# Kernel optimization log

Measured on AMD Instinct MI355X. Metric: run time of the kernel, lower is better.

## Reference

```python
import jax, jax.numpy as jnp
import numpy as np

HEADS = 8
DIM_HEAD = 128
ATTN_MATRIX_SCALE = 1.5  # tau applied to mean-centered logits
SCALE = DIM_HEAD ** -0.5


def setup_inputs() -> dict:
    key = jax.random.key(0)
    ks = jax.random.split(key, 7)
    b, n, m = 2, 2048, 2048
    qd, cd, inner = 1024, 768, HEADS * DIM_HEAD
    x = jax.random.normal(ks[0], (b, n, qd), dtype=jnp.float32)
    context = jax.random.normal(ks[1], (b, m, cd), dtype=jnp.float32)
    Wq = jax.random.normal(ks[2], (qd, inner), dtype=jnp.float32) * (qd ** -0.5)
    Wk = jax.random.normal(ks[3], (cd, inner), dtype=jnp.float32) * (cd ** -0.5)
    Wv = jax.random.normal(ks[4], (cd, inner), dtype=jnp.float32) * (cd ** -0.5)
    Wout = jax.random.normal(ks[5], (inner, qd), dtype=jnp.float32) * (inner ** -0.5)
    bout = jnp.zeros((qd,), dtype=jnp.float32)
    return {"x": x, "context": context, "Wq": Wq, "Wk": Wk, "Wv": Wv,
            "Wout": Wout, "bout": bout}


def _split_heads(t):
    # (b, n, h*d) -> (h, b*n, d); matches rearrange '(b h) n d -> h (b n) d'
    b, n, _ = t.shape
    t = t.reshape(b, n, HEADS, DIM_HEAD)
    return t.transpose(2, 0, 1, 3).reshape(HEADS, b * n, DIM_HEAD)


def reference(x, context, Wq, Wk, Wv, Wout, bout):
    b, n, _ = x.shape
    qh = _split_heads(jnp.einsum('bnq,qi->bni', x, Wq))        # (h, b*n, d)
    kh = _split_heads(jnp.einsum('bmc,ci->bmi', context, Wk))  # (h, b*m, d)
    vh = _split_heads(jnp.einsum('bmc,ci->bmi', context, Wv))  # (h, b*m, d)

    # custom mean-centered / tau-scaled similarity (_compute_sim_with_tau)
    sim = jnp.einsum('hid,hjd->hij', qh, kh) * SCALE
    mean = jnp.mean(sim, axis=-1, keepdims=True)
    sim = (sim - mean) * ATTN_MATRIX_SCALE + mean

    attn = jax.nn.softmax(sim, axis=-1)
    out = jnp.einsum('hij,hjd->hid', attn, vh)                 # (h, b*n, d)

    # (h, b*n, d) -> (b, n, h*d)
    out = out.reshape(HEADS, b, n, DIM_HEAD).transpose(1, 2, 0, 3)
    out = out.reshape(b, n, HEADS * DIM_HEAD)
    return jnp.einsum('bni,iq->bnq', out, Wout) + bout
```

## Files before the change

kernel.cpp:

```cpp
#include <hip/hip_runtime.h>
#include <cstdint>
#include <cstddef>

typedef unsigned short u16t;
typedef __bf16 bf16x8_t __attribute__((ext_vector_type(8)));
typedef float f32x4_t __attribute__((ext_vector_type(4)));
typedef float f32x16_t __attribute__((ext_vector_type(16)));

#define MFMA_BF16 __builtin_amdgcn_mfma_f32_16x16x32_bf16
#define MFMA32    __builtin_amdgcn_mfma_f32_32x32x16_bf16

__device__ __forceinline__ u16t f2bf(float f) {
    uint32_t u = __builtin_bit_cast(uint32_t, f);
    u += 0x7fffu + ((u >> 16) & 1u);
    return (u16t)(u >> 16);
}

__device__ __forceinline__ uint32_t pk2bf(float a, float b) {
    return (uint32_t)f2bf(a) | ((uint32_t)f2bf(b) << 16);
}

__device__ __forceinline__ float bflo(uint32_t u) {
    return __builtin_bit_cast(float, u << 16);
}
__device__ __forceinline__ float bfhi(uint32_t u) {
    return __builtin_bit_cast(float, u & 0xffff0000u);
}

__device__ __forceinline__ bf16x8_t ld_frag(const u16t* p) {
    return __builtin_bit_cast(bf16x8_t, *(const uint4*)p);
}

__device__ __forceinline__ uint32_t cvtpk(float lo, float hi) {
    uint32_t r;
    asm("v_cvt_pk_bf16_f32 %0, %1, %2" : "=v"(r) : "v"(lo), "v"(hi));
    return r;
}
__device__ __forceinline__ void swap32(uint32_t& a, uint32_t& b) {
    asm("v_permlane32_swap_b32 %0, %1" : "+v"(a), "+v"(b));
}

__device__ __forceinline__ void gl_lds16(const u16t* g, u16t* l) {
    __builtin_amdgcn_global_load_lds(
        (const __attribute__((address_space(1))) void*)g,
        (__attribute__((address_space(3))) void*)l, 16, 0, 0);
}

__global__ void cast2_bf16_kernel(const float* __restrict__ s0, u16t* __restrict__ d0, int n0,
                                  const float* __restrict__ s1, u16t* __restrict__ d1, int n1) {
    int i = blockIdx.x * blockDim.x + threadIdx.x;
    const float* s; u16t* d;
    if (i < n0) { s = s0; d = d0; }
    else { i -= n0; if (i >= n1) return; s = s1; d = d1; }
    float4 v = ((const float4*)s)[i];
    uint2 o;
    o.x = pk2bf(v.x, v.y);
    o.y = pk2bf(v.z, v.w);
    ((uint2*)d)[i] = o;
}

__global__ void transpose4_kernel(const float* __restrict__ Wq, const float* __restrict__ Wk,
                                  const float* __restrict__ Wv, const float* __restrict__ Wo,
                                  u16t* __restrict__ Wqt, u16t* __restrict__ Wkt,
                                  u16t* __restrict__ Wvt, u16t* __restrict__ Wot) {
    const int z = blockIdx.z;
    const float* W = z == 0 ? Wq : (z == 1 ? Wk : (z == 2 ? Wv : Wo));
    u16t* Wt      = z == 0 ? Wqt : (z == 1 ? Wkt : (z == 2 ? Wvt : Wot));
    const int K   = (z == 1 || z == 2) ? 768 : 1024;
    const int N = 1024;
    int n0 = blockIdx.x * 32, k0 = blockIdx.y * 32;
    if (k0 >= K) return;
    __shared__ float tile[32][33];
    int tx = threadIdx.x, ty = threadIdx.y;
    for (int i = ty; i < 32; i += 8)
        tile[i][tx] = W[(size_t)(k0 + i) * N + n0 + tx];
    __syncthreads();
    for (int i = ty; i < 32; i += 8)
        Wt[(size_t)(n0 + i) * K + k0 + tx] = f2bf(tile[tx][i]);
}

__device__ __forceinline__ void gemm_core(
    const u16t* __restrict__ A, const u16t* __restrict__ Bt,
    int K, void* __restrict__ outp, const float* __restrict__ bias,
    int mode, float oscale, int bm, int bn)
{
    __shared__ __align__(16) u16t As[2][128 * 64];
    __shared__ __align__(16) u16t Bs[2][64 * 64];
    const int tid = threadIdx.x;
    const int wave = tid >> 6, lane = tid & 63;
    const int wm = wave & 1, wn = wave >> 1;
    const int quad = lane >> 4, l16 = lane & 15;

    const int l8r = lane >> 3, l8c = lane & 7;
    const int cgx = (l8c ^ l8r) * 8;

    f32x4_t acc[4][2];
#pragma unroll
    for (int i = 0; i < 4; ++i)
#pragma unroll
        for (int j = 0; j < 2; ++j) acc[i][j] = (f32x4_t){0.f, 0.f, 0.f, 0.f};

    const int nk = K >> 6;

#pragma unroll
    for (int it = 0; it < 4; ++it) {
        int rb = wave * 32 + it * 8;
        gl_lds16(&A[(size_t)(bm + rb + l8r) * K + cgx], &As[0][rb * 64]);
    }
#pragma unroll
    for (int it = 0; it < 2; ++it) {
        int rb = wave * 16 + it * 8;
        gl_lds16(&Bt[(size_t)(bn + rb + l8r) * K + cgx], &Bs[0][rb * 64]);
    }

    for (int ki = 0; ki < nk; ++ki) {
        const int buf = ki & 1;
        __syncthreads();

        if (ki + 1 < nk) {
            const int kc = (ki + 1) << 6;
#pragma unroll
            for (int it = 0; it < 4; ++it) {
                int rb = wave * 32 + it * 8;
                gl_lds16(&A[(size_t)(bm + rb + l8r) * K + kc + cgx], &As[buf ^ 1][rb * 64]);
            }
#pragma unroll
            for (int it = 0; it < 2; ++it) {
                int rb = wave * 16 + it * 8;
                gl_lds16(&Bt[(size_t)(bn + rb + l8r) * K + kc + cgx], &Bs[buf ^ 1][rb * 64]);
            }
        }

#pragma unroll
        for (int ks = 0; ks < 2; ++ks) {
            bf16x8_t af[4], bfv[2];
#pragma unroll
            for (int i = 0; i < 4; ++i) {
                int r = wm * 64 + i * 16 + l16;
                af[i] = ld_frag(&As[buf][r * 64 + (((ks * 4 + quad) ^ (r & 7)) * 8)]);
            }
#pragma unroll
            for (int j = 0; j < 2; ++j) {
                int r = wn * 32 + j * 16 + l16;
                bfv[j] = ld_frag(&Bs[buf][r * 64 + (((ks * 4 + quad) ^ (r & 7)) * 8)]);
            }
#pragma unroll
            for (int i = 0; i < 4; ++i)
#pragma unroll
                for (int j = 0; j < 2; ++j)
                    acc[i][j] = MFMA_BF16(af[i], bfv[j], acc[i][j], 0, 0, 0);
        }
    }

    if (mode == 3) {
        float* out = (float*)outp;
#pragma unroll
        for (int j = 0; j < 2; ++j) {
            int c = bn + wn * 32 + j * 16 + l16;
            float b = bias[c];
#pragma unroll
            for (int i = 0; i < 4; ++i) {
                int rb = bm + wm * 64 + i * 16 + quad * 4;
#pragma unroll
                for (int r = 0; r < 4; ++r)
                    out[(size_t)(rb + r) * 1024 + c] = acc[i][j][r] + b;
            }
        }
    }
}

__global__ __launch_bounds__(256) void gemm_bf16_kernel(
    const u16t* __restrict__ A, const u16t* __restrict__ Bt,
    int K, void* __restrict__ outp, const float* __restrict__ bias,
    int mode, float oscale)
{
    gemm_core(A, Bt, K, outp, bias, mode, oscale, blockIdx.y * 128, blockIdx.x * 64);
}

__global__ __launch_bounds__(256, 2) void qkv128_kernel(
    const u16t* __restrict__ x_bf, const u16t* __restrict__ ctx_bf,
    const u16t* __restrict__ Wqt, const u16t* __restrict__ Wkt,
    const u16t* __restrict__ Wvt,
    u16t* __restrict__ Qh, u16t* __restrict__ Kh, u16t* __restrict__ Vt,
    float qscale)
{
    extern __shared__ __align__(16) u16t sm[];
    const int z = blockIdx.z;
    const u16t* A  = (z == 0) ? x_bf : ctx_bf;
    const u16t* Bt = (z == 0) ? Wqt : ((z == 1) ? Wkt : Wvt);
    const int K    = (z == 0) ? 1024 : 768;
    const float sc = (z == 0) ? qscale : 1.0f;
    const int m0 = blockIdx.y * 128;
    const int h  = blockIdx.x;

    const int tid = threadIdx.x;
    const int wave = tid >> 6, lane = tid & 63;
    const int l31 = lane & 31, hh = lane >> 5;
    const int wm = wave & 1, wn = wave >> 1;
    const bool aRole = wave < 2;
    const int wh = wave & 1;
    const int rS = lane >> 3, cS = lane & 7;

    const int nk = K >> 6;
    const u16t* G  = aRole ? A : Bt;
    const int base = aRole ? m0 : h * 128;
    u16t* dstb     = sm + (aRole ? 0 : 16384);

#pragma unroll
    for (int it = 0; it < 8; ++it) {
        int is = wh * 8 + it;
        int rowL = is * 8 + rS;
        gl_lds16(&G[(size_t)(base + rowL) * K + ((cS ^ ((rowL ^ (rowL >> 3)) & 7)) * 8)],
                 dstb + is * 512);
    }

    f32x16_t acc[2][2];
#pragma unroll
    for (int i = 0; i < 2; ++i)
#pragma unroll
        for (int j = 0; j < 2; ++j)
#pragma unroll
            for (int r = 0; r < 16; ++r) acc[i][j][r] = 0.f;

    for (int ki = 0; ki < nk; ++ki) {
        const int buf = ki & 1;
        __syncthreads();

        if (ki + 1 < nk) {
            const int kc = (ki + 1) << 6;
            u16t* dst = dstb + (buf ^ 1) * 8192;
#pragma unroll
            for (int it = 0; it < 8; ++it) {
                int is = wh * 8 + it;
                int rowL = is * 8 + rS;
                gl_lds16(&G[(size_t)(base + rowL) * K + kc + ((cS ^ ((rowL ^ (rowL >> 3)) & 7)) * 8)],
                         dst + is * 512);
            }
        }

        const u16t* As = sm + buf * 8192;
        const u16t* Bs = sm + 16384 + buf * 8192;
        __builtin_amdgcn_s_setprio(1);
#pragma unroll
        for (int s = 0; s < 4; ++s) {
            bf16x8_t af[2], bfr[2];
#pragma unroll
            for (int i = 0; i < 2; ++i) {
                int r = wm * 64 + i * 32 + l31;
                af[i] = ld_frag(&As[r * 64 + (((s * 2 + hh) ^ ((r ^ (r >> 3)) & 7)) * 8)]);
            }
#pragma unroll
            for (int j = 0; j < 2; ++j) {
                int r = wn * 64 + j * 32 + l31;
                bfr[j] = ld_frag(&Bs[r * 64 + (((s * 2 + hh) ^ ((r ^ (r >> 3)) & 7)) * 8)]);
            }
#pragma unroll
            for (int i = 0; i < 2; ++i)
#pragma unroll
                for (int j = 0; j < 2; ++j)
                    acc[i][j] = MFMA32(af[i], bfr[j], acc[i][j], 0, 0, 0);
        }
        __builtin_amdgcn_s_setprio(0);
    }

    if (z != 2) {
        u16t* out = (z == 0) ? Qh : Kh;
#pragma unroll
        for (int i = 0; i < 2; ++i)
#pragma unroll
            for (int j = 0; j < 2; ++j) {
                int d = wn * 64 + j * 32 + l31;
#pragma unroll
                for (int g = 0; g < 16; ++g) {
                    int m = m0 + wm * 64 + i * 32 + (g & 3) + 8 * (g >> 2) + 4 * hh;
                    out[((size_t)h * 4096 + m) * 128 + d] = f2bf(acc[i][j][g] * sc);
                }
            }
    } else {
#pragma unroll
        for (int i = 0; i < 2; ++i)
#pragma unroll
            for (int j = 0; j < 2; ++j) {
                int d = wn * 64 + j * 32 + l31;
                size_t vb = ((size_t)h * 128 + d) * 4096 + m0 + wm * 64 + i * 32;
#pragma unroll
                for (int gq = 0; gq < 4; ++gq) {
                    uint2 pk;
                    pk.x = pk2bf(acc[i][j][gq * 4 + 0], acc[i][j][gq * 4 + 1]);
                    pk.y = pk2bf(acc[i][j][gq * 4 + 2], acc[i][j][gq * 4 + 3]);
                    *(uint2*)&Vt[vb + gq * 8 + 4 * hh] = pk;
                }
            }
    }
}

__global__ __launch_bounds__(256, 2) void flash_kernel(
    const u16t* __restrict__ Qh, const u16t* __restrict__ Kh,
    const u16t* __restrict__ Vtg, u16t* __restrict__ Op0,
    u16t* __restrict__ Op1, float* __restrict__ lp)
{
    extern __shared__ __align__(16) u16t smem[];
    const int h = blockIdx.y;
    const int q0 = blockIdx.x * 128;
    const int z = blockIdx.z;
    const int tid = threadIdx.x;
    const int wave = tid >> 6, lane = tid & 63;
    const int l31 = lane & 31, hh = lane >> 5;
    const int NT = 32;

    const u16t* Kg = Kh + (size_t)h * 4096 * 128 + (size_t)z * 2048 * 128;
    const u16t* Vg = Vtg + (size_t)h * 128 * 4096 + z * 2048;

    {
        const u16t* Qg = Qh + ((size_t)h * 4096 + q0) * 128;
#pragma unroll
        for (int it = 0; it < 8; ++it) {
            int slot = it * 256 + tid;
            int r = slot >> 4, c = slot & 15;
            uint4 v = *(const uint4*)&Qg[(size_t)r * 128 + c * 8];
            *(uint4*)&smem[r * 128 + ((c ^ (r & 15)) * 8)] = v;
        }
    }
    __syncthreads();
    bf16x8_t qf[8];
    {
        int r = wave * 32 + l31;
#pragma unroll
        for (int s = 0; s < 8; ++s)
            qf[s] = ld_frag(&smem[r * 128 + (((s * 2 + hh) ^ (r & 15)) * 8)]);
    }
    __syncthreads();

    const bool kRole = wave < 2;
    const int wh = wave & 1;
    const int rK = lane >> 4, cK = lane & 15;
    const int rV = lane >> 3, cV = lane & 7;

    if (kRole) {
#pragma unroll
        for (int it = 0; it < 8; ++it) {
            int is = wh * 8 + it;
            int rowL = is * 4 + rK;
            gl_lds16(Kg + (size_t)rowL * 128 + ((cK ^ (rowL & 15)) * 8),
                     smem + is * 512);
        }
    }

    f32x16_t Ow[4];
#pragma unroll
    for (int dg = 0; dg < 4; ++dg)
#pragma unroll
        for (int r = 0; r < 16; ++r) Ow[dg][r] = 0.f;

    float lsum = 0.f;
    const int swzk = l31 & 15;
    bf16x8_t pf[4];

    for (int t = 0; t <= NT; ++t) {
        __syncthreads();

        if (kRole) {
            if (t + 1 < NT) {
                const int j0 = (t + 1) * 64;
                u16t* kd = smem + ((t + 1) & 1) * 8192;
#pragma unroll
                for (int it = 0; it < 8; ++it) {
                    int is = wh * 8 + it;
                    int rowL = is * 4 + rK;
                    gl_lds16(Kg + (size_t)(j0 + rowL) * 128 + ((cK ^ (rowL & 15)) * 8),
                             kd + is * 512);
                }
            }
        } else {
            if (t < NT) {
                const int j0 = t * 64;
                u16t* vd = smem + 16384 + (t & 1) * 8192;
#pragma unroll
                for (int it = 0; it < 8; ++it) {
                    int is = wh * 8 + it;
                    int rowL = is * 8 + rV;
                    gl_lds16(Vg + (size_t)rowL * 4096 + j0 + ((cV ^ ((rowL ^ (rowL >> 3)) & 7)) * 8),
                             vd + is * 512);
                }
            }
        }

        __builtin_amdgcn_s_setprio(1);
        f32x16_t St0, St1;
#pragma unroll
        for (int r = 0; r < 16; ++r) { St0[r] = 0.f; St1[r] = 0.f; }
        if (t < NT) {
            const u16t* kb = smem + (t & 1) * 8192;
#pragma unroll
            for (int s = 0; s < 8; ++s) {
                int ch = ((s * 2 + hh) ^ swzk) * 8;
                bf16x8_t k0 = ld_frag(&kb[l31 * 128 + ch]);
                bf16x8_t k1 = ld_frag(&kb[(32 + l31) * 128 + ch]);
                St0 = MFMA32(k0, qf[s], St0, 0, 0, 0);
                St1 = MFMA32(k1, qf[s], St1, 0, 0, 0);
            }
        }
        if (t >= 1) {
            const u16t* vb = smem + 16384 + ((t - 1) & 1) * 8192;
#pragma unroll
            for (int dg = 0; dg < 4; ++dg) {
                int rv = dg * 32 + l31;
                int gsw = (rv ^ (rv >> 3)) & 7;
#pragma unroll
                for (int sl = 0; sl < 4; ++sl) {
                    bf16x8_t vf = ld_frag(&vb[rv * 64 + (((sl * 2 + hh) ^ gsw) * 8)]);
                    Ow[dg] = MFMA32(vf, pf[sl], Ow[dg], 0, 0, 0);
                }
            }
        }
        __builtin_amdgcn_s_setprio(0);

        if (t < NT) {
#pragma unroll
            for (int half = 0; half < 2; ++half) {
                float p[16];
#pragma unroll
                for (int r = 0; r < 16; ++r)
                    p[r] = __builtin_amdgcn_exp2f(half ? St1[r] : St0[r]);
                lsum += ((((p[0] + p[1]) + (p[2] + p[3])) + ((p[4] + p[5]) + (p[6] + p[7])))
                      + (((p[8] + p[9]) + (p[10] + p[11])) + ((p[12] + p[13]) + (p[14] + p[15]))));
                uint32_t w0 = cvtpk(p[0], p[1]),   w2 = cvtpk(p[4], p[5]);
                uint32_t w1 = cvtpk(p[2], p[3]),   w3 = cvtpk(p[6], p[7]);
                swap32(w0, w2); swap32(w1, w3);
                uint32_t y0 = cvtpk(p[8], p[9]),   y2 = cvtpk(p[12], p[13]);
                uint32_t y1 = cvtpk(p[10], p[11]), y3 = cvtpk(p[14], p[15]);
                swap32(y0, y2); swap32(y1, y3);
                uint4 pw0; pw0.x = w0; pw0.y = w1; pw0.z = w2; pw0.w = w3;
                uint4 pw1; pw1.x = y0; pw1.y = y1; pw1.z = y2; pw1.w = y3;
                pf[half * 2 + 0] = __builtin_bit_cast(bf16x8_t, pw0);
                pf[half * 2 + 1] = __builtin_bit_cast(bf16x8_t, pw1);
            }
        }
    }

    lsum += __shfl_xor(lsum, 32, 64);
    u16t* Op = z ? Op1 : Op0;
    size_t i = (size_t)(q0 + wave * 32 + l31);
    if (hh == 0) lp[z * 32768 + i * 8 + h] = lsum;
#pragma unroll
    for (int dg = 0; dg < 4; ++dg)
#pragma unroll
        for (int g = 0; g < 4; ++g) {
            uint2 pk;
            pk.x = pk2bf(Ow[dg][g * 4 + 0], Ow[dg][g * 4 + 1]);
            pk.y = pk2bf(Ow[dg][g * 4 + 2], Ow[dg][g * 4 + 3]);
            *(uint2*)&Op[i * 1024 + h * 128 + dg * 32 + g * 8 + hh * 4] = pk;
        }
}

__global__ __launch_bounds__(256) void combine_kernel(
    const u16t* __restrict__ O0, const u16t* __restrict__ O1,
    const float* __restrict__ lp, u16t* __restrict__ out)
{
    int t = blockIdx.x * blockDim.x + threadIdx.x;
    int e = t << 3;
    int i = e >> 10, h = (e >> 7) & 7;
    float inv = 1.f / (lp[i * 8 + h] + lp[32768 + i * 8 + h]);
    uint4 a = ((const uint4*)O0)[t];
    uint4 b = ((const uint4*)O1)[t];
    uint4 r;
    r.x = pk2bf((bflo(a.x) + bflo(b.x)) * inv, (bfhi(a.x) + bfhi(b.x)) * inv);
    r.y = pk2bf((bflo(a.y) + bflo(b.y)) * inv, (bfhi(a.y) + bfhi(b.y)) * inv);
    r.z = pk2bf((bflo(a.z) + bflo(b.z)) * inv, (bfhi(a.z) + bfhi(b.z)) * inv);
    r.w = pk2bf((bflo(a.w) + bflo(b.w)) * inv, (bfhi(a.w) + bfhi(b.w)) * inv);
    ((uint4*)out)[t] = r;
}

extern "C" void kernel_launch(void* const* d_in, const int* in_sizes, int n_in,
                              void* d_out, int out_size, void* d_ws, size_t ws_size,
                              hipStream_t stream)
{
    (void)in_sizes; (void)n_in; (void)out_size; (void)ws_size;
    const float* x    = (const float*)d_in[0];
    const float* ctx  = (const float*)d_in[1];
    const float* Wq   = (const float*)d_in[2];
    const float* Wk   = (const float*)d_in[3];
    const float* Wv   = (const float*)d_in[4];
    const float* Wout = (const float*)d_in[5];
    const float* bout = (const float*)d_in[6];
    float* out = (float*)d_out;

    u16t* ws = (u16t*)d_ws;
    u16t* x_bf   = ws;
    u16t* ctx_bf = x_bf + 4194304;
    u16t* Wqt    = ctx_bf + 3145728;
    u16t* Wkt    = Wqt + 1048576;
    u16t* Wvt    = Wkt + 786432;
    u16t* Woutt  = Wvt + 786432;
    u16t* Qh     = Woutt + 1048576;
    u16t* Kh     = Qh + 4194304;
    u16t* Vt     = Kh + 4194304;
    u16t* Oh   = x_bf;
    u16t* Ohp1 = ws + 4194304;
    float* lp  = (float*)(ws + 8388608);

    constexpr float QSCALE = 1.5f * 0.08838834764831845f * 1.4426950408889634f;

    (void)hipFuncSetAttribute((const void*)flash_kernel,
                              hipFuncAttributeMaxDynamicSharedMemorySize, 65536);
    (void)hipFuncSetAttribute((const void*)qkv128_kernel,
                              hipFuncAttributeMaxDynamicSharedMemorySize, 65536);

    cast2_bf16_kernel<<<7168, 256, 0, stream>>>(x, x_bf, 1048576, ctx, ctx_bf, 786432);
    transpose4_kernel<<<dim3(32, 32, 4), dim3(32, 8), 0, stream>>>(
        Wq, Wk, Wv, Wout, Wqt, Wkt, Wvt, Woutt);

    qkv128_kernel<<<dim3(8, 32, 3), 256, 65536, stream>>>(
        x_bf, ctx_bf, Wqt, Wkt, Wvt, Qh, Kh, Vt, QSCALE);

    flash_kernel<<<dim3(32, 8, 2), 256, 65536, stream>>>(Qh, Kh, Vt, Oh, Ohp1, lp);
    combine_kernel<<<2048, 256, 0, stream>>>(Oh, Ohp1, lp, Oh);

    gemm_bf16_kernel<<<dim3(16, 32), 256, 0, stream>>>(Oh, Woutt, 1024, out, bout, 3, 1.0f);
}
```

Before: 229.6 us.

## Replace output projection GEMM with 128x128-tile 32x32 MFMA kernel

Result: slower. 238.3 us (+3.8%).

```diff
diff --git a/kernel.cpp b/kernel.cpp
--- a/kernel.cpp
+++ b/kernel.cpp
@@ -7,8 +7,7 @@
 typedef float f32x4_t __attribute__((ext_vector_type(4)));
 typedef float f32x16_t __attribute__((ext_vector_type(16)));
 
-#define MFMA_BF16 __builtin_amdgcn_mfma_f32_16x16x32_bf16
-#define MFMA32    __builtin_amdgcn_mfma_f32_32x32x16_bf16
+#define MFMA32 __builtin_amdgcn_mfma_f32_32x32x16_bf16
 
 __device__ __forceinline__ u16t f2bf(float f) {
     uint32_t u = __builtin_bit_cast(uint32_t, f);
@@ -79,104 +78,6 @@
         Wt[(size_t)(n0 + i) * K + k0 + tx] = f2bf(tile[tx][i]);
 }
 
-__device__ __forceinline__ void gemm_core(
-    const u16t* __restrict__ A, const u16t* __restrict__ Bt,
-    int K, void* __restrict__ outp, const float* __restrict__ bias,
-    int mode, float oscale, int bm, int bn)
-{
-    __shared__ __align__(16) u16t As[2][128 * 64];
-    __shared__ __align__(16) u16t Bs[2][64 * 64];
-    const int tid = threadIdx.x;
-    const int wave = tid >> 6, lane = tid & 63;
-    const int wm = wave & 1, wn = wave >> 1;
-    const int quad = lane >> 4, l16 = lane & 15;
-
-    const int l8r = lane >> 3, l8c = lane & 7;
-    const int cgx = (l8c ^ l8r) * 8;
-
-    f32x4_t acc[4][2];
-#pragma unroll
-    for (int i = 0; i < 4; ++i)
-#pragma unroll
-        for (int j = 0; j < 2; ++j) acc[i][j] = (f32x4_t){0.f, 0.f, 0.f, 0.f};
-
-    const int nk = K >> 6;
-
-#pragma unroll
-    for (int it = 0; it < 4; ++it) {
-        int rb = wave * 32 + it * 8;
-        gl_lds16(&A[(size_t)(bm + rb + l8r) * K + cgx], &As[0][rb * 64]);
-    }
-#pragma unroll
-    for (int it = 0; it < 2; ++it) {
-        int rb = wave * 16 + it * 8;
-        gl_lds16(&Bt[(size_t)(bn + rb + l8r) * K + cgx], &Bs[0][rb * 64]);
-    }
-
-    for (int ki = 0; ki < nk; ++ki) {
-        const int buf = ki & 1;
-        __syncthreads();
-
-        if (ki + 1 < nk) {
-            const int kc = (ki + 1) << 6;
-#pragma unroll
-            for (int it = 0; it < 4; ++it) {
-                int rb = wave * 32 + it * 8;
-                gl_lds16(&A[(size_t)(bm + rb + l8r) * K + kc + cgx], &As[buf ^ 1][rb * 64]);
-            }
-#pragma unroll
-            for (int it = 0; it < 2; ++it) {
-                int rb = wave * 16 + it * 8;
-                gl_lds16(&Bt[(size_t)(bn + rb + l8r) * K + kc + cgx], &Bs[buf ^ 1][rb * 64]);
-            }
-        }
-
-#pragma unroll
-        for (int ks = 0; ks < 2; ++ks) {
-            bf16x8_t af[4], bfv[2];
-#pragma unroll
-            for (int i = 0; i < 4; ++i) {
-                int r = wm * 64 + i * 16 + l16;
-                af[i] = ld_frag(&As[buf][r * 64 + (((ks * 4 + quad) ^ (r & 7)) * 8)]);
-            }
-#pragma unroll
-            for (int j = 0; j < 2; ++j) {
-                int r = wn * 32 + j * 16 + l16;
-                bfv[j] = ld_frag(&Bs[buf][r * 64 + (((ks * 4 + quad) ^ (r & 7)) * 8)]);
-            }
-#pragma unroll
-            for (int i = 0; i < 4; ++i)
-#pragma unroll
-                for (int j = 0; j < 2; ++j)
-                    acc[i][j] = MFMA_BF16(af[i], bfv[j], acc[i][j], 0, 0, 0);
-        }
-    }
-
-    if (mode == 3) {
-        float* out = (float*)outp;
-#pragma unroll
-        for (int j = 0; j < 2; ++j) {
-            int c = bn + wn * 32 + j * 16 + l16;
-            float b = bias[c];
-#pragma unroll
-            for (int i = 0; i < 4; ++i) {
-                int rb = bm + wm * 64 + i * 16 + quad * 4;
-#pragma unroll
-                for (int r = 0; r < 4; ++r)
-                    out[(size_t)(rb + r) * 1024 + c] = acc[i][j][r] + b;
-            }
-        }
-    }
-}
-
-__global__ __launch_bounds__(256) void gemm_bf16_kernel(
-    const u16t* __restrict__ A, const u16t* __restrict__ Bt,
-    int K, void* __restrict__ outp, const float* __restrict__ bias,
-    int mode, float oscale)
-{
-    gemm_core(A, Bt, K, outp, bias, mode, oscale, blockIdx.y * 128, blockIdx.x * 64);
-}
-
 __global__ __launch_bounds__(256, 2) void qkv128_kernel(
     const u16t* __restrict__ x_bf, const u16t* __restrict__ ctx_bf,
     const u16t* __restrict__ Wqt, const u16t* __restrict__ Wkt,
@@ -292,6 +193,83 @@
                 }
             }
     }
+}
+
+__global__ __launch_bounds__(512, 2) void gemm_out_kernel(
+    const u16t* __restrict__ A, const u16t* __restrict__ Bt,
+    float* __restrict__ out, const float* __restrict__ bias)
+{
+    extern __shared__ __align__(16) u16t sm[];
+    const int K = 1024, nk = 16;
+    const int m0 = blockIdx.y * 128, n0 = blockIdx.x * 128;
+    const int tid = threadIdx.x;
+    const int wave = tid >> 6, lane = tid & 63;
+    const int l31 = lane & 31, hh = lane >> 5;
+    const int wm = wave & 1, wn = wave >> 1;
+    const bool aRole = wave < 4;
+    const int wq = wave & 3;
+    const int rS = lane >> 3, cS = lane & 7;
+
+    const u16t* G  = aRole ? A : Bt;
+    const int base = aRole ? m0 : n0;
+    u16t* dstb     = sm + (aRole ? 0 : 16384);
+
+#pragma unroll
+    for (int it = 0; it < 4; ++it) {
+        int is = wq * 4 + it;
+        int rowL = is * 8 + rS;
+        gl_lds16(&G[(size_t)(base + rowL) * K + ((cS ^ ((rowL ^ (rowL >> 3)) & 7)) * 8)],
+                 dstb + is * 512);
+    }
+
+    f32x16_t acc[2];
+#pragma unroll
+    for (int i = 0; i < 2; ++i)
+#pragma unroll
+        for (int r = 0; r < 16; ++r) acc[i][r] = 0.f;
+
+    for (int ki = 0; ki < nk; ++ki) {
+        const int buf = ki & 1;
+        __syncthreads();
+
+        if (ki + 1 < nk) {
+            const int kc = (ki + 1) << 6;
+            u16t* dst = dstb + (buf ^ 1) * 8192;
+#pragma unroll
+            for (int it = 0; it < 4; ++it) {
+                int is = wq * 4 + it;
+                int rowL = is * 8 + rS;
+                gl_lds16(&G[(size_t)(base + rowL) * K + kc + ((cS ^ ((rowL ^ (rowL >> 3)) & 7)) * 8)],
+                         dst + is * 512);
+            }
+        }
+
+        const u16t* As = sm + buf * 8192;
+        const u16t* Bs = sm + 16384 + buf * 8192;
+        __builtin_amdgcn_s_setprio(1);
+#pragma unroll
+        for (int s = 0; s < 4; ++s) {
+            int rb = wn * 32 + l31;
+            bf16x8_t bfr = ld_frag(&Bs[rb * 64 + (((s * 2 + hh) ^ ((rb ^ (rb >> 3)) & 7)) * 8)]);
+#pragma unroll
+            for (int i = 0; i < 2; ++i) {
+                int ra = wm * 64 + i * 32 + l31;
+                bf16x8_t af = ld_frag(&As[ra * 64 + (((s * 2 + hh) ^ ((ra ^ (ra >> 3)) & 7)) * 8)]);
+                acc[i] = MFMA32(af, bfr, acc[i], 0, 0, 0);
+            }
+        }
+        __builtin_amdgcn_s_setprio(0);
+    }
+
+    const int c = n0 + wn * 32 + l31;
+    const float b = bias[c];
+#pragma unroll
+    for (int i = 0; i < 2; ++i)
+#pragma unroll
+        for (int g = 0; g < 16; ++g) {
+            int m = m0 + wm * 64 + i * 32 + (g & 3) + 8 * (g >> 2) + 4 * hh;
+            out[(size_t)m * 1024 + c] = acc[i][g] + b;
+        }
 }
 
 __global__ __launch_bounds__(256, 2) void flash_kernel(
@@ -505,6 +483,8 @@
                               hipFuncAttributeMaxDynamicSharedMemorySize, 65536);
     (void)hipFuncSetAttribute((const void*)qkv128_kernel,
                               hipFuncAttributeMaxDynamicSharedMemorySize, 65536);
+    (void)hipFuncSetAttribute((const void*)gemm_out_kernel,
+                              hipFuncAttributeMaxDynamicSharedMemorySize, 65536);
 
     cast2_bf16_kernel<<<7168, 256, 0, stream>>>(x, x_bf, 1048576, ctx, ctx_bf, 786432);
     transpose4_kernel<<<dim3(32, 32, 4), dim3(32, 8), 0, stream>>>(
@@ -516,5 +496,5 @@
     flash_kernel<<<dim3(32, 8, 2), 256, 65536, stream>>>(Qh, Kh, Vt, Oh, Ohp1, lp);
     combine_kernel<<<2048, 256, 0, stream>>>(Oh, Ohp1, lp, Oh);
 
-    gemm_bf16_kernel<<<dim3(16, 32), 256, 0, stream>>>(Oh, Woutt, 1024, out, bout, 3, 1.0f);
-}
+    gemm_out_kernel<<<dim3(8, 32), 512, 65536, stream>>>(Oh, Woutt, out, bout);
+}
```
